# Kernel optimization log

Measured on AMD Instinct MI355X. Metric: run time of the kernel, lower is better.

Reference implementation:

```python
import jax, jax.numpy as jnp
import numpy as np

B, C, H, W = 32, 1024, 32, 32  # N = H*W must equal C for the attn_c * attn_s broadcast
C8 = C // 8


def setup_inputs() -> dict:
    key = jax.random.key(0)
    ks = jax.random.split(key, 9)
    s = 1.0 / np.sqrt(C)
    return {
        "z": jax.random.normal(ks[0], (B, C, H, W), jnp.float32),
        "x": jax.random.normal(ks[1], (B, C, H, W), jnp.float32),
        "y": jax.random.normal(ks[2], (B, C, H, W), jnp.float32),
        "Wq": jax.random.normal(ks[3], (C8, C), jnp.float32) * s,
        "bq": jax.random.normal(ks[4], (C8,), jnp.float32) * 0.01,
        "Wk": jax.random.normal(ks[5], (C8, C), jnp.float32) * s,
        "bk": jax.random.normal(ks[6], (C8,), jnp.float32) * 0.01,
        "Wv": jax.random.normal(ks[7], (C, C), jnp.float32) * s,
        "bv": jax.random.normal(ks[8], (C,), jnp.float32) * 0.01,
    }


def reference(z, x, y, Wq, bq, Wk, bk, Wv, bv):
    b, c, h, w = x.shape
    n = h * w
    xf = x.reshape(b, c, n)
    yf = y.reshape(b, c, n)
    zf = z.reshape(b, c, n)

    # 1x1 convs == channel matmuls
    q = jnp.einsum('oc,bcn->bon', Wq, xf) + bq[None, :, None]   # (B, C/8, N)
    k = jnp.einsum('oc,bcn->bon', Wk, yf) + bk[None, :, None]   # (B, C/8, N)

    # channel-projected spatial attention: (B, N, N)
    energy_c = jnp.einsum('bcn,bcm->bnm', q, k)
    attention_c = jax.nn.softmax(energy_c, axis=-1)

    # raw channel attention: (B, C, C)
    energy_s = jnp.einsum('bcn,bdn->bcd', xf, yf)
    energy_s = jnp.max(energy_s, axis=-1, keepdims=True) - energy_s
    attention_s = jax.nn.softmax(energy_s, axis=-1)

    # multiplicative combine + third softmax (requires N == C)
    attention = jax.nn.softmax(attention_c * attention_s, axis=-1)

    v = jnp.einsum('oc,bcn->bon', Wv, zf) + bv[None, :, None]   # (B, C, N)
    # out[b,c,m] = sum_n v[b,c,n] * attention[b,m,n]  (value @ attention^T)
    out = jnp.einsum('bcn,bmn->bcm', v, attention)
    return z + out.reshape(b, c, h, w)
```

## Files before the change

### kernel.cpp

```cpp
#include <hip/hip_runtime.h>
#include <hip/hip_bf16.h>

typedef __attribute__((ext_vector_type(8))) short s8_t;
typedef __attribute__((ext_vector_type(4))) float f4_t;

__device__ __forceinline__ unsigned short f2bf(float f) {
  union { float f; unsigned u; } x; x.f = f;
  unsigned r = x.u + 0x7fffu + ((x.u >> 16) & 1u);
  return (unsigned short)(r >> 16);
}

__device__ __forceinline__ void split1(float v, unsigned short& h, unsigned short& l) {
  unsigned b = __float_as_uint(v);
  unsigned hb = b & 0xFFFF0000u;
  h = (unsigned short)(b >> 16);
  float lo = v - __uint_as_float(hb);
  l = (unsigned short)(__float_as_uint(lo) >> 16);
}

__device__ __forceinline__ void split2(float e0, float e1, unsigned& hp, unsigned& lp) {
  unsigned b0 = __float_as_uint(e0), b1 = __float_as_uint(e1);
  unsigned h0 = b0 & 0xFFFF0000u, h1 = b1 & 0xFFFF0000u;
  hp = (b0 >> 16) | h1;
  float l0 = e0 - __uint_as_float(h0), l1 = e1 - __uint_as_float(h1);
  lp = (__float_as_uint(l0) >> 16) | (__float_as_uint(l1) & 0xFFFF0000u);
}

__device__ __forceinline__ void gload16(const void* g, void* l) {
  __builtin_amdgcn_global_load_lds(
      (const __attribute__((address_space(1))) void*)g,
      (__attribute__((address_space(3))) void*)l, 16, 0, 0);
}

__device__ __forceinline__ void swz_grid(int& bx, int& by, int& bz) {
  const int gx = gridDim.x, gy = gridDim.y;
  const int nwg = gx * gy * gridDim.z;
  const int flat = (blockIdx.z * gy + blockIdx.y) * gx + blockIdx.x;
  const int s = (flat & 7) * (nwg >> 3) + (flat >> 3);
  bx = s % gx;
  const int r = s / gx;
  by = r % gy;
  bz = r / gy;
}

__global__ __launch_bounds__(256) void k_convert(const float* __restrict__ in,
                                                 unsigned short* __restrict__ out, int n) {
  int i = (blockIdx.x * 256 + threadIdx.x) * 8;
  if (i >= n) return;
  float4 a = *(const float4*)(in + i);
  float4 b = *(const float4*)(in + i + 4);
  ushort4 u0; u0.x = f2bf(a.x); u0.y = f2bf(a.y); u0.z = f2bf(a.z); u0.w = f2bf(a.w);
  ushort4 u1; u1.x = f2bf(b.x); u1.y = f2bf(b.y); u1.z = f2bf(b.z); u1.w = f2bf(b.w);
  *(ushort4*)(out + i) = u0;
  *(ushort4*)(out + i + 4) = u1;
}

__global__ __launch_bounds__(256) void k_tsplitT(const float* __restrict__ in,
                                                 unsigned short* __restrict__ th,
                                                 unsigned short* __restrict__ tl) {
  __shared__ float tile[64][65];
  const int t = threadIdx.x, bz = blockIdx.z;
  const int r0 = blockIdx.y * 64, c0 = blockIdx.x * 64;
  const float* ip = in + (size_t)bz * 1048576;
  const size_t ob = (size_t)bz * 1048576;
  const int tr = t >> 4, tc = (t & 15) * 4;
#pragma unroll
  for (int p = 0; p < 4; ++p) {
    int r = p * 16 + tr;
    float4 v = *(const float4*)(ip + (size_t)(r0 + r) * 1024 + c0 + tc);
    tile[r][tc] = v.x; tile[r][tc + 1] = v.y; tile[r][tc + 2] = v.z; tile[r][tc + 3] = v.w;
  }
  __syncthreads();
#pragma unroll
  for (int p = 0; p < 4; ++p) {
    int n = p * 16 + tr;
    float a = tile[tc][n], b = tile[tc + 1][n], c = tile[tc + 2][n], d = tile[tc + 3][n];
    ushort4 h, l;
    split1(a, h.x, l.x); split1(b, h.y, l.y); split1(c, h.z, l.z); split1(d, h.w, l.w);
    *(ushort4*)(th + ob + (size_t)(c0 + n) * 1024 + r0 + tc) = h;
    *(ushort4*)(tl + ob + (size_t)(c0 + n) * 1024 + r0 + tc) = l;
  }
}

__global__ __launch_bounds__(256) void k_transpbf(const float* __restrict__ in,
                                                  unsigned short* __restrict__ outt) {
  __shared__ unsigned short tile[64][72];
  const int t = threadIdx.x, b = blockIdx.z;
  const int r0 = blockIdx.y * 64, c0 = blockIdx.x * 64;
  const float* ip = in + (size_t)b * 1048576;
  const int tr = t >> 4, tc = (t & 15) * 4;
#pragma unroll
  for (int p = 0; p < 4; ++p) {
    int r = p * 16 + tr;
    float4 v = *(const float4*)(ip + (size_t)(r0 + r) * 1024 + c0 + tc);
    tile[r][tc] = f2bf(v.x); tile[r][tc + 1] = f2bf(v.y);
    tile[r][tc + 2] = f2bf(v.z); tile[r][tc + 3] = f2bf(v.w);
  }
  __syncthreads();
#pragma unroll
  for (int p = 0; p < 4; ++p) {
    int n = p * 16 + tr;
    ushort4 w;
    w.x = tile[tc][n]; w.y = tile[tc + 1][n]; w.z = tile[tc + 2][n]; w.w = tile[tc + 3][n];
    *(ushort4*)(outt + (size_t)b * 1048576 + (size_t)(c0 + n) * 1024 + r0 + tc) = w;
  }
}

__device__ __forceinline__ void split_write_swz(unsigned short* buf, int w0, int w1,
                                                const float* av, const float* bv) {
  unsigned ah[8], al[8], bh[8], bl[8];
#pragma unroll
  for (int p = 0; p < 8; ++p) {
    split2(av[2 * p], av[2 * p + 1], ah[p], al[p]);
    split2(bv[2 * p], bv[2 * p + 1], bh[p], bl[p]);
  }
  *(uint4*)(buf + w0) = *(uint4*)(ah);
  *(uint4*)(buf + w1) = *(uint4*)(ah + 4);
  *(uint4*)(buf + 4096 + w0) = *(uint4*)(al);
  *(uint4*)(buf + 4096 + w1) = *(uint4*)(al + 4);
  *(uint4*)(buf + 8192 + w0) = *(uint4*)(bh);
  *(uint4*)(buf + 8192 + w1) = *(uint4*)(bh + 4);
  *(uint4*)(buf + 12288 + w0) = *(uint4*)(bl);
  *(uint4*)(buf + 12288 + w1) = *(uint4*)(bl + 4);
}

template <int BIAS_MODE>
__global__ __launch_bounds__(256) void k_mfma3(
    const float* __restrict__ A, int lda, long long sA,
    const float* __restrict__ B, int ldb, long long sB,
    float* __restrict__ C, int ldc, long long sC,
    const float* __restrict__ bias, int K) {
  __shared__ __align__(16) unsigned short sm[16384];
  int bxs, bys, bz; swz_grid(bxs, bys, bz);
  const int tid = threadIdx.x;
  const int lane = tid & 63, wave = tid >> 6;
  const int wr = wave >> 1, wc = wave & 1;
  const int m0 = bxs * 128, n0 = bys * 128;

  const int sr = tid >> 1, sh = (tid & 1) * 16;
  const float* ag = A + (long long)bz * sA + (long long)(m0 + sr) * lda + sh;
  const float* bg = B + (long long)bz * sB + (long long)(n0 + sr) * ldb + sh;
  const int swm = (sr >> 1) & 3;
  const int s0 = (tid & 1) * 2;
  const int w0 = sr * 32 + (s0 ^ swm) * 8;
  const int w1 = sr * 32 + ((s0 + 1) ^ swm) * 8;

  const int lr = lane & 15, lg = lane >> 4;
  const int rdm = (lr >> 1) & 3;
  const int fa = (wr * 64 + lr) * 32 + (lg ^ rdm) * 8;
  const int fb = (wc * 64 + lr) * 32 + (lg ^ rdm) * 8;

  f4_t acc[4][4];
#pragma unroll
  for (int i = 0; i < 4; ++i)
#pragma unroll
    for (int j = 0; j < 4; ++j) acc[i][j] = (f4_t)0.f;

  for (int k0 = 0; k0 < K; k0 += 32) {
    float av[16], bv[16];
#pragma unroll
    for (int p = 0; p < 4; ++p) {
      *(float4*)(av + p * 4) = *(const float4*)(ag + p * 4);
      *(float4*)(bv + p * 4) = *(const float4*)(bg + p * 4);
    }
    split_write_swz(sm, w0, w1, av, bv);
    ag += 32; bg += 32;
    __syncthreads();
    const unsigned short* Ahp = sm;
    const unsigned short* Alp = sm + 4096;
    const unsigned short* Bhp = sm + 8192;
    const unsigned short* Blp = sm + 12288;
    s8_t fah[4], fbh[4], ftmp[4];
#pragma unroll
    for (int f = 0; f < 4; ++f) {
      fah[f] = *(const s8_t*)(Ahp + fa + f * 512);
      fbh[f] = *(const s8_t*)(Bhp + fb + f * 512);
    }
#pragma unroll
    for (int i = 0; i < 4; ++i)
#pragma unroll
      for (int j = 0; j < 4; ++j)
        acc[i][j] = __builtin_amdgcn_mfma_f32_16x16x32_bf16(fah[i], fbh[j], acc[i][j], 0, 0, 0);
#pragma unroll
    for (int f = 0; f < 4; ++f) ftmp[f] = *(const s8_t*)(Blp + fb + f * 512);
#pragma unroll
    for (int i = 0; i < 4; ++i)
#pragma unroll
      for (int j = 0; j < 4; ++j)
        acc[i][j] = __builtin_amdgcn_mfma_f32_16x16x32_bf16(fah[i], ftmp[j], acc[i][j], 0, 0, 0);
#pragma unroll
    for (int f = 0; f < 4; ++f) ftmp[f] = *(const s8_t*)(Alp + fa + f * 512);
#pragma unroll
    for (int i = 0; i < 4; ++i)
#pragma unroll
      for (int j = 0; j < 4; ++j)
        acc[i][j] = __builtin_amdgcn_mfma_f32_16x16x32_bf16(ftmp[i], fbh[j], acc[i][j], 0, 0, 0);
    __syncthreads();
  }

#pragma unroll
  for (int i = 0; i < 4; ++i) {
    const int rbase = m0 + wr * 64 + i * 16 + lg * 4;
#pragma unroll
    for (int j = 0; j < 4; ++j) {
      const int col = n0 + wc * 64 + j * 16 + lr;
      float bc = (BIAS_MODE == 2) ? bias[col] : 0.f;
#pragma unroll
      for (int e = 0; e < 4; ++e) {
        float v = acc[i][j][e];
        if (BIAS_MODE == 2) v += bc;
        C[(long long)bz * sC + (long long)(rbase + e) * ldc + col] = v;
      }
    }
  }
}

__global__ __launch_bounds__(256) void k_qk3p(
    const unsigned short* __restrict__ Axh, const unsigned short* __restrict__ Axl,
    const unsigned short* __restrict__ Ayh, const unsigned short* __restrict__ Ayl,
    const float* __restrict__ Wqf, const float* __restrict__ Wkf,
    const float* __restrict__ bqf, const float* __restrict__ bkf,
    float* __restrict__ Qt, float* __restrict__ Kt) {
  __shared__ __align__(16) unsigned short smAh[8192], smAl[8192];
  __shared__ __align__(16) unsigned short smBh[4096], smBl[4096];
  int bx, by, bz; swz_grid(bx, by, bz);
  const unsigned short* Ah = by ? Ayh : Axh;
  const unsigned short* Al = by ? Ayl : Axl;
  const float* Bf = by ? Wkf : Wqf;
  const float* bias = by ? bkf : bqf;
  float* Of = by ? Kt : Qt;

  const int tid = threadIdx.x, lane = tid & 63, wave = tid >> 6;
  const int wr = wave >> 1, wc = wave & 1;
  const int m0 = bx * 128;

  const int ch0 = wave * 64 + lane, ch1 = ch0 + 256;
  const int r0 = ch0 >> 2, kc0 = (((ch0 & 3) ^ ((ch0 >> 3) & 3))) * 8;
  const int r1 = ch1 >> 2, kc1 = (((ch1 & 3) ^ ((ch1 >> 3) & 3))) * 8;
  const unsigned short* pah0 = Ah + (long long)bz * 1048576 + (long long)(m0 + r0) * 1024 + kc0;
  const unsigned short* pah1 = Ah + (long long)bz * 1048576 + (long long)(m0 + r1) * 1024 + kc1;
  const unsigned short* pal0 = Al + (long long)bz * 1048576 + (long long)(m0 + r0) * 1024 + kc0;
  const unsigned short* pal1 = Al + (long long)bz * 1048576 + (long long)(m0 + r1) * 1024 + kc1;

  const int sr = tid >> 1, sh = (tid & 1) * 16;
  const float* bg = Bf + (long long)sr * 1024 + sh;
  const int swm = (sr >> 1) & 3;
  const int sB0 = (tid & 1) * 2;
  const int w0 = sr * 32 + (sB0 ^ swm) * 8;
  const int w1 = sr * 32 + ((sB0 + 1) ^ swm) * 8;

  const int lr = lane & 15, lg = lane >> 4;
  const int rdm = (lr >> 1) & 3;
  const int fa = (wr * 64 + lr) * 32 + (lg ^ rdm) * 8;
  const int fb = (wc * 64 + lr) * 32 + (lg ^ rdm) * 8;

  f4_t acc[4][4];
#pragma unroll
  for (int i = 0; i < 4; ++i)
#pragma unroll
    for (int j = 0; j < 4; ++j) acc[i][j] = (f4_t)0.f;

  float bv[16];
  auto stageA = [&](int b) {
    char* dh = (char*)smAh + b * 8192 + wave * 1024;
    char* dl = (char*)smAl + b * 8192 + wave * 1024;
    gload16(pah0, dh); gload16(pah1, dh + 4096);
    gload16(pal0, dl); gload16(pal1, dl + 4096);
    pah0 += 32; pah1 += 32; pal0 += 32; pal1 += 32;
  };
  auto loadW = [&]() {
#pragma unroll
    for (int p = 0; p < 4; ++p) *(float4*)(bv + p * 4) = *(const float4*)(bg + p * 4);
    bg += 32;
  };
  auto writeW = [&]() {
    unsigned bh[8], bl[8];
#pragma unroll
    for (int p = 0; p < 8; ++p) split2(bv[2 * p], bv[2 * p + 1], bh[p], bl[p]);
    *(uint4*)(smBh + w0) = *(uint4*)(bh);
    *(uint4*)(smBh + w1) = *(uint4*)(bh + 4);
    *(uint4*)(smBl + w0) = *(uint4*)(bl);
    *(uint4*)(smBl + w1) = *(uint4*)(bl + 4);
  };

  stageA(0);
  loadW();
  writeW();
  asm volatile("s_waitcnt vmcnt(0)" ::: "memory");
  __builtin_amdgcn_sched_barrier(0);
  __builtin_amdgcn_s_barrier();
  __builtin_amdgcn_sched_barrier(0);

  for (int t = 0; t < 32; ++t) {
    const bool more = (t < 31);
    if (more) { stageA((t + 1) & 1); loadW(); }
    const unsigned short* Ahp = smAh + (t & 1) * 4096;
    const unsigned short* Alp = smAl + (t & 1) * 4096;
    s8_t fah[4], fbh[4], ft[4];
#pragma unroll
    for (int f = 0; f < 4; ++f) {
      fah[f] = *(const s8_t*)(Ahp + fa + f * 512);
      fbh[f] = *(const s8_t*)(smBh + fb + f * 512);
    }
#pragma unroll
    for (int i = 0; i < 4; ++i)
#pragma unroll
      for (int j = 0; j < 4; ++j)
        acc[i][j] = __builtin_amdgcn_mfma_f32_16x16x32_bf16(fah[i], fbh[j], acc[i][j], 0, 0, 0);
#pragma unroll
    for (int f = 0; f < 4; ++f) ft[f] = *(const s8_t*)(smBl + fb + f * 512);
#pragma unroll
    for (int i = 0; i < 4; ++i)
#pragma unroll
      for (int j = 0; j < 4; ++j)
        acc[i][j] = __builtin_amdgcn_mfma_f32_16x16x32_bf16(fah[i], ft[j], acc[i][j], 0, 0, 0);
#pragma unroll
    for (int f = 0; f < 4; ++f) ft[f] = *(const s8_t*)(Alp + fa + f * 512);
#pragma unroll
    for (int i = 0; i < 4; ++i)
#pragma unroll
      for (int j = 0; j < 4; ++j)
        acc[i][j] = __builtin_amdgcn_mfma_f32_16x16x32_bf16(ft[i], fbh[j], acc[i][j], 0, 0, 0);
    __builtin_amdgcn_sched_barrier(0);
    __builtin_amdgcn_s_barrier();
    __builtin_amdgcn_sched_barrier(0);
    if (more) {
      writeW();
      asm volatile("s_waitcnt vmcnt(0)" ::: "memory");
    }
    __builtin_amdgcn_sched_barrier(0);
    __builtin_amdgcn_s_barrier();
    __builtin_amdgcn_sched_barrier(0);
  }

#pragma unroll
  for (int i = 0; i < 4; ++i) {
    const int rbase = m0 + wr * 64 + i * 16 + lg * 4;
#pragma unroll
    for (int j = 0; j < 4; ++j) {
      const int col = wc * 64 + j * 16 + lr;
      const float bc = bias[col];
#pragma unroll
      for (int e = 0; e < 4; ++e)
        Of[(long long)bz * 131072 + (long long)(rbase + e) * 128 + col] = acc[i][j][e] + bc;
    }
  }
}

template <int BIAS_MODE, bool OUT_BF16, bool RESID>
__global__ __launch_bounds__(512) void k_mfma256(
    const unsigned short* __restrict__ A, int lda, long long sA,
    const unsigned short* __restrict__ B, int ldb, long long sB,
    void* __restrict__ Cp, int ldc, long long sC,
    const float* __restrict__ bias,
    const float* __restrict__ resid, long long sR, int K) {
  __shared__ __align__(16) unsigned short As[32768];
  __shared__ __align__(16) unsigned short Bs[32768];
  int bxs, bys, bz; swz_grid(bxs, bys, bz);
  const int tid = threadIdx.x;
  const int lane = tid & 63, wave = tid >> 6;
  const int wr = wave >> 2, wc = wave & 3;
  const int m0 = bxs * 256, n0 = bys * 256;

  const int cA0 = tid, cA1 = tid + 512;
  const int rr0 = cA0 >> 2, sl0 = ((cA0 & 3) ^ ((cA0 >> 3) & 3)) * 8;
  const int rr1 = cA1 >> 2, sl1 = ((cA1 & 3) ^ ((cA1 >> 3) & 3)) * 8;
  const unsigned short* pa0 = A + (long long)bz * sA + (long long)(m0 + rr0) * lda + sl0;
  const unsigned short* pa1 = A + (long long)bz * sA + (long long)(m0 + rr1) * lda + sl1;
  const unsigned short* pb0 = B + (long long)bz * sB + (long long)(n0 + rr0) * ldb + sl0;
  const unsigned short* pb1 = B + (long long)bz * sB + (long long)(n0 + rr1) * ldb + sl1;

  const int lr = lane & 15, lg = lane >> 4;
  const int rdm = (lr >> 1) & 3;
  const int fa = (wr * 128 + lr) * 32 + (lg ^ rdm) * 8;
  const int fb = (wc * 64 + lr) * 32 + (lg ^ rdm) * 8;

  f4_t acc[8][4];
#pragma unroll
  for (int i = 0; i < 8; ++i)
#pragma unroll
    for (int j = 0; j < 4; ++j) acc[i][j] = (f4_t)0.f;

  unsigned short* a0 = As;        unsigned short* a1 = As + 8192;
  unsigned short* a2 = As + 16384; unsigned short* a3 = As + 24576;
  unsigned short* b0 = Bs;        unsigned short* b1 = Bs + 8192;
  unsigned short* b2 = Bs + 16384; unsigned short* b3 = Bs + 24576;

  auto gA0 = [&](unsigned short* la) { gload16(pa0, (char*)la + wave * 1024); pa0 += 32; };
  auto gA1 = [&](unsigned short* la) { gload16(pa1, (char*)la + 8192 + wave * 1024); pa1 += 32; };
  auto gB0 = [&](unsigned short* lb) { gload16(pb0, (char*)lb + wave * 1024); pb0 += 32; };
  auto gB1 = [&](unsigned short* lb) { gload16(pb1, (char*)lb + 8192 + wave * 1024); pb1 += 32; };

  const int nt = K >> 5;
  gA0(a0); gA1(a0); gB0(b0); gB1(b0);
  gA0(a1); gA1(a1); gB0(b1); gB1(b1);
  gA0(a2); gA1(a2); gB0(b2); gB1(b2);

  for (int t = 0; t < nt; ++t) {
    const int rem = nt - 1 - t;
    if (rem >= 2)      asm volatile("s_waitcnt vmcnt(8)" ::: "memory");
    else if (rem == 1) asm volatile("s_waitcnt vmcnt(4)" ::: "memory");
    else               asm volatile("s_waitcnt vmcnt(0)" ::: "memory");
    __builtin_amdgcn_sched_barrier(0);
    __builtin_amdgcn_s_barrier();
    __builtin_amdgcn_sched_barrier(0);
    const bool pf = (t + 3 < nt);
    const unsigned short* ap = a0;
    const unsigned short* bp = b0;
    s8_t af[4], af2[4], bf[4];
    if (pf) gA0(a3);
#pragma unroll
    for (int j = 0; j < 4; ++j) bf[j] = *(const s8_t*)(bp + fb + j * 512);
    if (pf) gA1(a3);
#pragma unroll
    for (int i = 0; i < 4; ++i) af[i] = *(const s8_t*)(ap + fa + i * 512);
    if (pf) gB0(b3);
    __builtin_amdgcn_s_setprio(1);
#pragma unroll
    for (int i = 0; i < 4; ++i)
#pragma unroll
      for (int j = 0; j < 4; ++j)
        acc[i][j] = __builtin_amdgcn_mfma_f32_16x16x32_bf16(af[i], bf[j], acc[i][j], 0, 0, 0);
    __builtin_amdgcn_s_setprio(0);
    if (pf) gB1(b3);
#pragma unroll
    for (int i = 0; i < 4; ++i) af2[i] = *(const s8_t*)(ap + fa + (i + 4) * 512);
    __builtin_amdgcn_s_setprio(1);
#pragma unroll
    for (int i = 0; i < 4; ++i)
#pragma unroll
      for (int j = 0; j < 4; ++j)
        acc[i + 4][j] = __builtin_amdgcn_mfma_f32_16x16x32_bf16(af2[i], bf[j], acc[i + 4][j], 0, 0, 0);
    __builtin_amdgcn_s_setprio(0);
    unsigned short* ta = a0; a0 = a1; a1 = a2; a2 = a3; a3 = ta;
    unsigned short* tb = b0; b0 = b1; b1 = b2; b2 = b3; b3 = tb;
  }

#pragma unroll
  for (int i = 0; i < 8; ++i) {
    const int rbase = m0 + wr * 128 + i * 16 + lg * 4;
#pragma unroll
    for (int j = 0; j < 4; ++j) {
      const int col = n0 + wc * 64 + j * 16 + lr;
#pragma unroll
      for (int e = 0; e < 4; ++e) {
        const int row = rbase + e;
        float v = acc[i][j][e];
        if (BIAS_MODE == 1) v += bias[row];
        const long long off = (long long)bz * sC + (long long)row * ldc + col;
        if (RESID) v += resid[(long long)bz * sR + (long long)row * ldc + col];
        if (OUT_BF16) ((unsigned short*)Cp)[off] = f2bf(v);
        else          ((float*)Cp)[off] = v;
      }
    }
  }
}

__device__ __forceinline__ float wred_max(float v) {
#pragma unroll
  for (int o = 1; o < 64; o <<= 1) v = fmaxf(v, __shfl_xor(v, o, 64));
  return v;
}
__device__ __forceinline__ float wred_sum(float v) {
#pragma unroll
  for (int o = 1; o < 64; o <<= 1) v += __shfl_xor(v, o, 64);
  return v;
}

__global__ __launch_bounds__(256) void k_combine(float* __restrict__ ec,
                                                 const float* __restrict__ es) {
  const int lane = threadIdx.x & 63, wid = threadIdx.x >> 6;
  const size_t row = (size_t)blockIdx.x * 4 + wid;
  float* cp = ec + row * 1024;
  const float* sp = es + row * 1024;
  float4 c[4], s[4];
#pragma unroll
  for (int p = 0; p < 4; ++p) {
    c[p] = ((const float4*)cp)[lane * 4 + p];
    s[p] = ((const float4*)sp)[lane * 4 + p];
  }
  float mx = -3.4e38f;
#pragma unroll
  for (int p = 0; p < 4; ++p)
    mx = fmaxf(mx, fmaxf(fmaxf(c[p].x, c[p].y), fmaxf(c[p].z, c[p].w)));
  mx = wred_max(mx);
  float e[16], lsum = 0.f;
#pragma unroll
  for (int p = 0; p < 4; ++p) {
    e[4 * p]     = __expf(c[p].x - mx);
    e[4 * p + 1] = __expf(c[p].y - mx);
    e[4 * p + 2] = __expf(c[p].z - mx);
    e[4 * p + 3] = __expf(c[p].w - mx);
    lsum += e[4 * p] + e[4 * p + 1] + e[4 * p + 2] + e[4 * p + 3];
  }
  const float sc = wred_sum(lsum);
  float mt = -3.4e38f;
#pragma unroll
  for (int p = 0; p < 4; ++p)
    mt = fmaxf(mt, fmaxf(fmaxf(-s[p].x, -s[p].y), fmaxf(-s[p].z, -s[p].w)));
  mt = wred_max(mt);
  float f[16]; lsum = 0.f;
#pragma unroll
  for (int p = 0; p < 4; ++p) {
    f[4 * p]     = __expf(-s[p].x - mt);
    f[4 * p + 1] = __expf(-s[p].y - mt);
    f[4 * p + 2] = __expf(-s[p].z - mt);
    f[4 * p + 3] = __expf(-s[p].w - mt);
    lsum += f[4 * p] + f[4 * p + 1] + f[4 * p + 2] + f[4 * p + 3];
  }
  const float ss = wred_sum(lsum);
  const float rc = 1.f / sc, rs = 1.f / ss;
  float g[16]; lsum = 0.f;
#pragma unroll
  for (int q = 0; q < 16; ++q) {
    g[q] = __expf((e[q] * rc) * (f[q] * rs));
    lsum += g[q];
  }
  const float s3 = wred_sum(lsum);
  const float r3 = 1.f / s3;
#pragma unroll
  for (int p = 0; p < 4; ++p) {
    ushort4 o;
    o.x = f2bf(g[4 * p] * r3);     o.y = f2bf(g[4 * p + 1] * r3);
    o.z = f2bf(g[4 * p + 2] * r3); o.w = f2bf(g[4 * p + 3] * r3);
    ((ushort4*)cp)[lane * 4 + p] = o;
  }
}

extern "C" void kernel_launch(void* const* d_in, const int* in_sizes, int n_in,
                              void* d_out, int out_size, void* d_ws, size_t ws_size,
                              hipStream_t stream) {
  const float* z = (const float*)d_in[0];
  const float* x = (const float*)d_in[1];
  const float* y = (const float*)d_in[2];
  const float* Wq = (const float*)d_in[3];
  const float* bq = (const float*)d_in[4];
  const float* Wk = (const float*)d_in[5];
  const float* bk = (const float*)d_in[6];
  const float* Wv = (const float*)d_in[7];
  const float* bv = (const float*)d_in[8];
  float* out = (float*)d_out;

  char* ws = (char*)d_ws;
  unsigned short* yth = (unsigned short*)ws;
  unsigned short* ytl = yth + 33554432;
  float* es = (float*)ws;
  unsigned short* z_t = (unsigned short*)ws;
  unsigned short* v_bf = z_t + 33554432;
  char* wsB = ws + 134217728;
  unsigned short* xth = (unsigned short*)wsB;
  unsigned short* xtl = xth + 33554432;
  float* ec = (float*)wsB;
  unsigned short* attn = (unsigned short*)wsB;
  char* wsC = ws + 268435456;
  float* q_t = (float*)wsC;
  float* k_t = q_t + 4194304;
  unsigned short* wv = (unsigned short*)wsC;

  dim3 blk(256);
  hipLaunchKernelGGL(k_tsplitT, dim3(16, 16, 32), blk, 0, stream, x, xth, xtl);
  hipLaunchKernelGGL(k_tsplitT, dim3(16, 16, 32), blk, 0, stream, y, yth, ytl);
  hipLaunchKernelGGL(k_qk3p, dim3(8, 2, 32), blk, 0, stream,
                     xth, xtl, yth, ytl, Wq, Wk, bq, bk, q_t, k_t);
  hipLaunchKernelGGL((k_mfma3<0>), dim3(8, 8, 32), blk, 0, stream,
                     x, 1024, 1048576LL, y, 1024, 1048576LL, es, 1024, 1048576LL,
                     (const float*)nullptr, 1024);
  hipLaunchKernelGGL((k_mfma3<0>), dim3(8, 8, 32), blk, 0, stream,
                     q_t, 128, 131072LL, k_t, 128, 131072LL, ec, 1024, 1048576LL,
                     (const float*)nullptr, 128);
  hipLaunchKernelGGL(k_combine, dim3(8192), blk, 0, stream, ec, es);
  hipLaunchKernelGGL(k_transpbf, dim3(16, 16, 32), blk, 0, stream, z, z_t);
  hipLaunchKernelGGL(k_convert, dim3(512), blk, 0, stream, Wv, wv, 1048576);
  hipLaunchKernelGGL((k_mfma256<1, true, false>), dim3(4, 4, 32), dim3(512), 0, stream,
                     wv, 1024, 0LL, z_t, 1024, 1048576LL, (void*)v_bf, 1024, 1048576LL,
                     bv, (const float*)nullptr, 0LL, 1024);
  hipLaunchKernelGGL((k_mfma256<0, false, true>), dim3(4, 4, 32), dim3(512), 0, stream,
                     v_bf, 1024, 1048576LL, attn, 2048, 2097152LL, (void*)out, 1024, 1048576LL,
                     (const float*)nullptr, z, 1048576LL, 1024);
}
```

Baseline: 765.3 us.

## Shrink mfma256 tile to 256x128 with triple-buffered LDS for higher occupancy

Reworks the big bf16 GEMM kernel used for the value projection and the attention-apply GEMM. The block tile goes from 256x256 to 256x128, the wave grid from 2x4 to 4x2, and the LDS ring from four stages to three, with fewer accumulators. Launch bounds now request 4 blocks and the grid doubles in N. The aim is to cut LDS and register use so more blocks fit per CU and latency is better hidden. In exchange, each block reuses its A tile across fewer columns and the prefetch depth drops.

```diff
diff --git a/kernel.cpp b/kernel.cpp
--- a/kernel.cpp
+++ b/kernel.cpp
@@ -348,73 +348,68 @@
 }
 
 template <int BIAS_MODE, bool OUT_BF16, bool RESID>
-__global__ __launch_bounds__(512) void k_mfma256(
+__global__ __launch_bounds__(512, 4) void k_mfma256(
     const unsigned short* __restrict__ A, int lda, long long sA,
     const unsigned short* __restrict__ B, int ldb, long long sB,
     void* __restrict__ Cp, int ldc, long long sC,
     const float* __restrict__ bias,
     const float* __restrict__ resid, long long sR, int K) {
-  __shared__ __align__(16) unsigned short As[32768];
-  __shared__ __align__(16) unsigned short Bs[32768];
+  __shared__ __align__(16) unsigned short As[24576];
+  __shared__ __align__(16) unsigned short Bs[12288];
   int bxs, bys, bz; swz_grid(bxs, bys, bz);
   const int tid = threadIdx.x;
   const int lane = tid & 63, wave = tid >> 6;
-  const int wr = wave >> 2, wc = wave & 3;
-  const int m0 = bxs * 256, n0 = bys * 256;
+  const int wr = wave >> 1, wc = wave & 1;
+  const int m0 = bxs * 256, n0 = bys * 128;
 
   const int cA0 = tid, cA1 = tid + 512;
-  const int rr0 = cA0 >> 2, sl0 = ((cA0 & 3) ^ ((cA0 >> 3) & 3)) * 8;
-  const int rr1 = cA1 >> 2, sl1 = ((cA1 & 3) ^ ((cA1 >> 3) & 3)) * 8;
-  const unsigned short* pa0 = A + (long long)bz * sA + (long long)(m0 + rr0) * lda + sl0;
-  const unsigned short* pa1 = A + (long long)bz * sA + (long long)(m0 + rr1) * lda + sl1;
-  const unsigned short* pb0 = B + (long long)bz * sB + (long long)(n0 + rr0) * ldb + sl0;
-  const unsigned short* pb1 = B + (long long)bz * sB + (long long)(n0 + rr1) * ldb + sl1;
+  const int ra0 = cA0 >> 2, sa0 = ((cA0 & 3) ^ ((cA0 >> 3) & 3)) * 8;
+  const int ra1 = cA1 >> 2, sa1 = ((cA1 & 3) ^ ((cA1 >> 3) & 3)) * 8;
+  const unsigned short* pa0 = A + (long long)bz * sA + (long long)(m0 + ra0) * lda + sa0;
+  const unsigned short* pa1 = A + (long long)bz * sA + (long long)(m0 + ra1) * lda + sa1;
+  const unsigned short* pb0 = B + (long long)bz * sB + (long long)(n0 + ra0) * ldb + sa0;
 
   const int lr = lane & 15, lg = lane >> 4;
   const int rdm = (lr >> 1) & 3;
-  const int fa = (wr * 128 + lr) * 32 + (lg ^ rdm) * 8;
+  const int fa = (wr * 64 + lr) * 32 + (lg ^ rdm) * 8;
   const int fb = (wc * 64 + lr) * 32 + (lg ^ rdm) * 8;
 
-  f4_t acc[8][4];
-#pragma unroll
-  for (int i = 0; i < 8; ++i)
+  f4_t acc[4][4];
+#pragma unroll
+  for (int i = 0; i < 4; ++i)
 #pragma unroll
     for (int j = 0; j < 4; ++j) acc[i][j] = (f4_t)0.f;
 
   unsigned short* a0 = As;        unsigned short* a1 = As + 8192;
-  unsigned short* a2 = As + 16384; unsigned short* a3 = As + 24576;
-  unsigned short* b0 = Bs;        unsigned short* b1 = Bs + 8192;
-  unsigned short* b2 = Bs + 16384; unsigned short* b3 = Bs + 24576;
+  unsigned short* a2 = As + 16384;
+  unsigned short* b0 = Bs;        unsigned short* b1 = Bs + 4096;
+  unsigned short* b2 = Bs + 8192;
 
   auto gA0 = [&](unsigned short* la) { gload16(pa0, (char*)la + wave * 1024); pa0 += 32; };
   auto gA1 = [&](unsigned short* la) { gload16(pa1, (char*)la + 8192 + wave * 1024); pa1 += 32; };
   auto gB0 = [&](unsigned short* lb) { gload16(pb0, (char*)lb + wave * 1024); pb0 += 32; };
-  auto gB1 = [&](unsigned short* lb) { gload16(pb1, (char*)lb + 8192 + wave * 1024); pb1 += 32; };
 
   const int nt = K >> 5;
-  gA0(a0); gA1(a0); gB0(b0); gB1(b0);
-  gA0(a1); gA1(a1); gB0(b1); gB1(b1);
-  gA0(a2); gA1(a2); gB0(b2); gB1(b2);
+  gA0(a0); gA1(a0); gB0(b0);
+  gA0(a1); gA1(a1); gB0(b1);
 
   for (int t = 0; t < nt; ++t) {
-    const int rem = nt - 1 - t;
-    if (rem >= 2)      asm volatile("s_waitcnt vmcnt(8)" ::: "memory");
-    else if (rem == 1) asm volatile("s_waitcnt vmcnt(4)" ::: "memory");
-    else               asm volatile("s_waitcnt vmcnt(0)" ::: "memory");
+    if (t < nt - 1) asm volatile("s_waitcnt vmcnt(3)" ::: "memory");
+    else            asm volatile("s_waitcnt vmcnt(0)" ::: "memory");
     __builtin_amdgcn_sched_barrier(0);
     __builtin_amdgcn_s_barrier();
     __builtin_amdgcn_sched_barrier(0);
-    const bool pf = (t + 3 < nt);
+    const bool pf = (t + 2 < nt);
     const unsigned short* ap = a0;
     const unsigned short* bp = b0;
-    s8_t af[4], af2[4], bf[4];
-    if (pf) gA0(a3);
+    s8_t af[4], bf[4];
+    if (pf) gA0(a2);
 #pragma unroll
     for (int j = 0; j < 4; ++j) bf[j] = *(const s8_t*)(bp + fb + j * 512);
-    if (pf) gA1(a3);
+    if (pf) gA1(a2);
 #pragma unroll
     for (int i = 0; i < 4; ++i) af[i] = *(const s8_t*)(ap + fa + i * 512);
-    if (pf) gB0(b3);
+    if (pf) gB0(b2);
     __builtin_amdgcn_s_setprio(1);
 #pragma unroll
     for (int i = 0; i < 4; ++i)
@@ -422,23 +417,13 @@
       for (int j = 0; j < 4; ++j)
         acc[i][j] = __builtin_amdgcn_mfma_f32_16x16x32_bf16(af[i], bf[j], acc[i][j], 0, 0, 0);
     __builtin_amdgcn_s_setprio(0);
-    if (pf) gB1(b3);
-#pragma unroll
-    for (int i = 0; i < 4; ++i) af2[i] = *(const s8_t*)(ap + fa + (i + 4) * 512);
-    __builtin_amdgcn_s_setprio(1);
-#pragma unroll
-    for (int i = 0; i < 4; ++i)
-#pragma unroll
-      for (int j = 0; j < 4; ++j)
-        acc[i + 4][j] = __builtin_amdgcn_mfma_f32_16x16x32_bf16(af2[i], bf[j], acc[i + 4][j], 0, 0, 0);
-    __builtin_amdgcn_s_setprio(0);
-    unsigned short* ta = a0; a0 = a1; a1 = a2; a2 = a3; a3 = ta;
-    unsigned short* tb = b0; b0 = b1; b1 = b2; b2 = b3; b3 = tb;
-  }
-
-#pragma unroll
-  for (int i = 0; i < 8; ++i) {
-    const int rbase = m0 + wr * 128 + i * 16 + lg * 4;
+    unsigned short* ta = a0; a0 = a1; a1 = a2; a2 = ta;
+    unsigned short* tb = b0; b0 = b1; b1 = b2; b2 = tb;
+  }
+
+#pragma unroll
+  for (int i = 0; i < 4; ++i) {
+    const int rbase = m0 + wr * 64 + i * 16 + lg * 4;
 #pragma unroll
     for (int j = 0; j < 4; ++j) {
       const int col = n0 + wc * 64 + j * 16 + lr;
@@ -571,10 +556,10 @@
   hipLaunchKernelGGL(k_combine, dim3(8192), blk, 0, stream, ec, es);
   hipLaunchKernelGGL(k_transpbf, dim3(16, 16, 32), blk, 0, stream, z, z_t);
   hipLaunchKernelGGL(k_convert, dim3(512), blk, 0, stream, Wv, wv, 1048576);
-  hipLaunchKernelGGL((k_mfma256<1, true, false>), dim3(4, 4, 32), dim3(512), 0, stream,
+  hipLaunchKernelGGL((k_mfma256<1, true, false>), dim3(4, 8, 32), dim3(512), 0, stream,
                      wv, 1024, 0LL, z_t, 1024, 1048576LL, (void*)v_bf, 1024, 1048576LL,
                      bv, (const float*)nullptr, 0LL, 1024);
-  hipLaunchKernelGGL((k_mfma256<0, false, true>), dim3(4, 4, 32), dim3(512), 0, stream,
+  hipLaunchKernelGGL((k_mfma256<0, false, true>), dim3(4, 8, 32), dim3(512), 0, stream,
                      v_bf, 1024, 1048576LL, attn, 2048, 2097152LL, (void*)out, 1024, 1048576LL,
                      (const float*)nullptr, z, 1048576LL, 1024);
 }
```

After: 746.7 us (median of 3 runs). -2.4%, faster.
